# Kernel optimization log

Measured on AMD Instinct MI355X. Metric: run time of the kernel, lower is better.

Reference implementation:

```python
import jax, jax.numpy as jnp
import numpy as np

DIM, EXP = 512, 16
INTERNAL = DIM * EXP  # 8192
BATCH, SEQ = 2, 2048


def setup_inputs() -> dict:
    key = jax.random.key(0)
    ks = jax.random.split(key, 8)
    s = 0.02
    return {
        "x": jax.random.normal(ks[0], (BATCH, SEQ, DIM), jnp.float32),
        "W_dt_w": jax.random.normal(ks[1], (INTERNAL, DIM), jnp.float32) * s,
        "W_dt_b": jnp.zeros((INTERNAL,), jnp.float32),
        "W_B_w": jax.random.normal(ks[2], (INTERNAL, DIM), jnp.float32) * s,
        "W_B_b": jnp.zeros((INTERNAL,), jnp.float32),
        "W_C_w": jax.random.normal(ks[3], (INTERNAL, DIM), jnp.float32) * s,
        "W_C_b": jnp.zeros((INTERNAL,), jnp.float32),
        "W_V_w": jax.random.normal(ks[4], (INTERNAL, DIM), jnp.float32) * s,
        "W_V_b": jnp.zeros((INTERNAL,), jnp.float32),
        # A_log = -rand(internal): negative for stability, as in torch init
        "A_log": -jax.random.uniform(ks[5], (INTERNAL,), jnp.float32),
        "W_out_w": jax.random.normal(ks[6], (DIM, INTERNAL), jnp.float32) * s,
        "W_out_b": jnp.zeros((DIM,), jnp.float32),
    }


def _scan_combine(c1, c2):
    # semi-separable recurrence h_t = a_t * h_{t-1} + b_t, as associative op
    a1, b1 = c1
    a2, b2 = c2
    return a2 * a1, a2 * b1 + b2


def reference(x, W_dt_w, W_dt_b, W_B_w, W_B_b, W_C_w, W_C_b,
              W_V_w, W_V_b, A_log, W_out_w, W_out_b):
    # Featurizer10: discretized SSM features. Shapes: x [b,s,d] -> [b,s,n]
    dt = jax.nn.softplus(jnp.einsum('bsd,nd->bsn', x, W_dt_w) + W_dt_b)
    A_bar = jnp.exp(dt * A_log)                                  # S: [b,s,n]
    B_bar = dt * (jnp.einsum('bsd,nd->bsn', x, W_B_w) + W_B_b)   # B: [b,s,n]
    C = jnp.einsum('bsd,nd->bsn', x, W_C_w) + W_C_b              # C: [b,s,n]
    V = jnp.einsum('bsd,nd->bsn', x, W_V_w) + W_V_b              # V: [b,s,n]
    # Token mixing: h_t = A_bar_t * h_{t-1} + B_bar_t * V_t (parallel scan)
    u = B_bar * V
    _, h = jax.lax.associative_scan(_scan_combine, (A_bar, u), axis=1)
    y = C * h                                                    # [b,s,n]
    # Output projection back to model dim
    return jnp.einsum('bsn,dn->bsd', y, W_out_w) + W_out_b
```

## Files before the change

### kernel.cpp

```cpp
#include <hip/hip_runtime.h>

#define DIMK 512
#define NCH  8192
#define MTOT 4096
#define SEQL 2048
#define KS   8

typedef __attribute__((ext_vector_type(8))) short bf16x8;
typedef __attribute__((ext_vector_type(4))) float f32x4;

__device__ __forceinline__ unsigned short f2bf(float f) {
  unsigned int u = __float_as_uint(f);
  u += 0x7fffu + ((u >> 16) & 1u);
  return (unsigned short)(u >> 16);
}
__device__ __forceinline__ float bf2f(unsigned short v) {
  return __uint_as_float(((unsigned int)v) << 16);
}

struct CvtArgs {
  const float* src[6];
  unsigned short* dst[6];
  int cum[7];
};
__global__ __launch_bounds__(256) void cvt_all_kernel(CvtArgs a, int tot) {
  const int stride = gridDim.x * 256;
  for (int i = blockIdx.x * 256 + threadIdx.x; i < tot; i += stride) {
    int s = 0;
    while (i >= a.cum[s + 1]) ++s;
    const int j = i - a.cum[s];
    const float4* sp = reinterpret_cast<const float4*>(a.src[s]);
    float4 v0 = sp[2 * j], v1 = sp[2 * j + 1];
    union { unsigned short us[8]; uint4 v; } o;
    o.us[0] = f2bf(v0.x); o.us[1] = f2bf(v0.y); o.us[2] = f2bf(v0.z); o.us[3] = f2bf(v0.w);
    o.us[4] = f2bf(v1.x); o.us[5] = f2bf(v1.y); o.us[6] = f2bf(v1.z); o.us[7] = f2bf(v1.w);
    reinterpret_cast<uint4*>(a.dst[s])[j] = o.v;
  }
}

__device__ __forceinline__ int swz(int row, int q) { return q ^ ((row >> 2) & 3); }

#define PLDS_A 4096
#define PLDS_W 8192
#define PLDS   (PLDS_A + PLDS_W)
__global__ __launch_bounds__(256) void proj_kernel(
    const unsigned short* __restrict__ xb,
    const unsigned short* __restrict__ w4,
    const float* __restrict__ b_dt, const float* __restrict__ b_B,
    const float* __restrict__ b_C, const float* __restrict__ b_V,
    const float* __restrict__ A_log,
    unsigned short* __restrict__ vlog,
    unsigned short* __restrict__ u_out,
    unsigned short* __restrict__ c_out)
{
  __shared__ __align__(16) unsigned short lds[3][PLDS];
  const int tid = threadIdx.x;
  const int lane = tid & 63;
  const int wave = tid >> 6;
  const int wr = wave >> 1, wc = wave & 1;
  const int n0 = blockIdx.x * 64;
  const int m0 = blockIdx.y * 128;

  auto stage = [&](int buf, int kt) {
    const int k0 = kt * 32;
    #pragma unroll
    for (int i = 0; i < 2; ++i) {
      int c = i * 256 + tid;
      int row = c >> 2, q = c & 3;
      const unsigned short* g = xb + (size_t)(m0 + row) * DIMK + k0 + swz(row, q) * 8;
      __builtin_amdgcn_global_load_lds(
          (const __attribute__((address_space(1))) void*)g,
          (__attribute__((address_space(3))) void*)&lds[buf][c * 8], 16, 0, 0);
    }
    #pragma unroll
    for (int p = 0; p < 4; ++p) {
      int row = tid >> 2, q = tid & 3;
      const unsigned short* g = w4 + ((size_t)p * NCH + n0 + row) * DIMK + k0 + swz(row, q) * 8;
      __builtin_amdgcn_global_load_lds(
          (const __attribute__((address_space(1))) void*)g,
          (__attribute__((address_space(3))) void*)&lds[buf][PLDS_A + p * 2048 + tid * 8], 16, 0, 0);
    }
  };

  f32x4 acc[4][4][2];
  #pragma unroll
  for (int p = 0; p < 4; ++p)
    #pragma unroll
    for (int fm = 0; fm < 4; ++fm)
      #pragma unroll
      for (int fn = 0; fn < 2; ++fn)
        acc[p][fm][fn] = (f32x4){0.f, 0.f, 0.f, 0.f};

  stage(0, 0);
  stage(1, 1);
  constexpr int NKT = DIMK / 32;
  #pragma unroll 1
  for (int kt = 0; kt < NKT; ++kt) {
    const int buf = kt % 3;
    if (kt < NKT - 1) asm volatile("s_waitcnt vmcnt(6)" ::: "memory");
    else              asm volatile("s_waitcnt vmcnt(0)" ::: "memory");
    __builtin_amdgcn_s_barrier();
    if (kt + 2 < NKT) stage((kt + 2) % 3, kt + 2);

    const int arow = wr * 64 + (lane & 15);
    const int qq = lane >> 4;
    bf16x8 af[4];
    #pragma unroll
    for (int fm = 0; fm < 4; ++fm) {
      const int r = arow + fm * 16;
      af[fm] = *reinterpret_cast<const bf16x8*>(&lds[buf][r * 32 + swz(r, qq) * 8]);
    }
    #pragma unroll
    for (int p = 0; p < 4; ++p) {
      bf16x8 bfr[2];
      #pragma unroll
      for (int fn = 0; fn < 2; ++fn) {
        const int r = wc * 32 + fn * 16 + (lane & 15);
        bfr[fn] = *reinterpret_cast<const bf16x8*>(
            &lds[buf][PLDS_A + p * 2048 + r * 32 + swz(r, qq) * 8]);
      }
      __builtin_amdgcn_s_setprio(1);
      #pragma unroll
      for (int fm = 0; fm < 4; ++fm)
        #pragma unroll
        for (int fn = 0; fn < 2; ++fn)
          acc[p][fm][fn] = __builtin_amdgcn_mfma_f32_16x16x32_bf16(
              af[fm], bfr[fn], acc[p][fm][fn], 0, 0, 0);
      __builtin_amdgcn_s_setprio(0);
    }
    asm volatile("s_waitcnt lgkmcnt(0)" ::: "memory");
  }

  #pragma unroll
  for (int fn = 0; fn < 2; ++fn) {
    const int n = n0 + wc * 32 + fn * 16 + (lane & 15);
    const float vbdt = b_dt[n], vbB = b_B[n], vbC = b_C[n], vbV = b_V[n];
    const float al = A_log[n];
    #pragma unroll
    for (int fm = 0; fm < 4; ++fm) {
      const int mbase = m0 + wr * 64 + fm * 16 + (lane >> 4) * 4;
      #pragma unroll
      for (int r = 0; r < 4; ++r) {
        const size_t off = (size_t)(mbase + r) * NCH + n;
        const float zdt = acc[0][fm][fn][r] + vbdt;
        const float zB  = acc[1][fm][fn][r] + vbB;
        const float zC  = acc[2][fm][fn][r] + vbC;
        const float zV  = acc[3][fm][fn][r] + vbV;
        const float dt = (zdt > 15.f) ? zdt : __logf(1.f + __expf(zdt));
        vlog[off]  = f2bf(dt * al);
        u_out[off] = f2bf(dt * zB * zV);
        c_out[off] = f2bf(zC);
      }
    }
  }
}

#define SCH 16
#define CSTEPS 128
__global__ __launch_bounds__(1024) void scan_kernel(
    const unsigned short* __restrict__ vlog,
    const unsigned short* __restrict__ u_in,
    unsigned short* cy)
{
  __shared__ float Ap[SCH][64], He[SCH][64], H0[SCH][64];
  const int lane = threadIdx.x & 63;
  const int w = threadIdx.x >> 6;
  const int c = blockIdx.x * 64 + lane;
  const size_t base = (size_t)blockIdx.y * SEQL * NCH + (size_t)(w * CSTEPS) * NCH + c;

  {
    const unsigned short* ap = vlog + base;
    const unsigned short* up = u_in + base;
    float h = 0.f, vsum = 0.f;
    #pragma unroll 1
    for (int s = 0; s < CSTEPS; s += 8) {
      float av[8], uv[8];
      #pragma unroll
      for (int i = 0; i < 8; ++i) {
        av[i] = bf2f(ap[(size_t)(s + i) * NCH]);
        uv[i] = bf2f(up[(size_t)(s + i) * NCH]);
      }
      #pragma unroll
      for (int i = 0; i < 8; ++i) {
        vsum += av[i];
        h = fmaf(__expf(av[i]), h, uv[i]);
      }
    }
    Ap[w][lane] = __expf(vsum);
    He[w][lane] = h;
  }
  __syncthreads();
  if (w == 0) {
    float run = 0.f;
    #pragma unroll
    for (int j = 0; j < SCH; ++j) {
      H0[j][lane] = run;
      run = fmaf(Ap[j][lane], run, He[j][lane]);
    }
  }
  __syncthreads();
  {
    const unsigned short* ap = vlog + base;
    const unsigned short* up = u_in + base;
    unsigned short* cp = cy + base;
    float h = H0[w][lane];
    #pragma unroll 1
    for (int s = 0; s < CSTEPS; s += 8) {
      float av[8], uv[8], cv[8];
      #pragma unroll
      for (int i = 0; i < 8; ++i) {
        av[i] = bf2f(ap[(size_t)(s + i) * NCH]);
        uv[i] = bf2f(up[(size_t)(s + i) * NCH]);
        cv[i] = bf2f(cp[(size_t)(s + i) * NCH]);
      }
      #pragma unroll
      for (int i = 0; i < 8; ++i) {
        h = fmaf(__expf(av[i]), h, uv[i]);
        cv[i] *= h;
      }
      #pragma unroll
      for (int i = 0; i < 8; ++i)
        __builtin_nontemporal_store(f2bf(cv[i]), &cp[(size_t)(s + i) * NCH]);
    }
  }
}

#define OLDS_A 4096
#define OLDS_B 2048
#define OLDS   (OLDS_A + OLDS_B)
__global__ __launch_bounds__(256) void outproj_kernel(
    const unsigned short* __restrict__ yb,
    const unsigned short* __restrict__ wout,
    float* __restrict__ partial)
{
  __shared__ __align__(16) unsigned short lds[3][OLDS];
  const int tid = threadIdx.x;
  const int lane = tid & 63;
  const int wave = tid >> 6;
  const int wr = wave >> 1, wc = wave & 1;
  const int m0 = blockIdx.x * 128;
  const int d0 = blockIdx.y * 64;
  const int kbase = blockIdx.z * (NCH / KS);

  auto stage = [&](int buf, int kt) {
    const int k0 = kbase + kt * 32;
    #pragma unroll
    for (int i = 0; i < 2; ++i) {
      int c = i * 256 + tid;
      int row = c >> 2, q = c & 3;
      const unsigned short* g = yb + (size_t)(m0 + row) * NCH + k0 + swz(row, q) * 8;
      __builtin_amdgcn_global_load_lds(
          (const __attribute__((address_space(1))) void*)g,
          (__attribute__((address_space(3))) void*)&lds[buf][c * 8], 16, 0, 0);
    }
    {
      int row = tid >> 2, q = tid & 3;
      const unsigned short* g = wout + (size_t)(d0 + row) * NCH + k0 + swz(row, q) * 8;
      __builtin_amdgcn_global_load_lds(
          (const __attribute__((address_space(1))) void*)g,
          (__attribute__((address_space(3))) void*)&lds[buf][OLDS_A + tid * 8], 16, 0, 0);
    }
  };

  f32x4 acc[4][2];
  #pragma unroll
  for (int fm = 0; fm < 4; ++fm)
    #pragma unroll
    for (int fn = 0; fn < 2; ++fn) acc[fm][fn] = (f32x4){0.f, 0.f, 0.f, 0.f};

  stage(0, 0);
  stage(1, 1);
  constexpr int NKT = (NCH / KS) / 32;
  #pragma unroll 1
  for (int kt = 0; kt < NKT; ++kt) {
    const int buf = kt % 3;
    if (kt < NKT - 1) asm volatile("s_waitcnt vmcnt(3)" ::: "memory");
    else              asm volatile("s_waitcnt vmcnt(0)" ::: "memory");
    __builtin_amdgcn_s_barrier();
    if (kt + 2 < NKT) stage((kt + 2) % 3, kt + 2);

    const int qq = lane >> 4;
    bf16x8 af[4], bfr[2];
    #pragma unroll
    for (int fm = 0; fm < 4; ++fm) {
      const int r = wr * 64 + fm * 16 + (lane & 15);
      af[fm] = *reinterpret_cast<const bf16x8*>(&lds[buf][r * 32 + swz(r, qq) * 8]);
    }
    #pragma unroll
    for (int fn = 0; fn < 2; ++fn) {
      const int r = wc * 32 + fn * 16 + (lane & 15);
      bfr[fn] = *reinterpret_cast<const bf16x8*>(
          &lds[buf][OLDS_A + r * 32 + swz(r, qq) * 8]);
    }
    __builtin_amdgcn_s_setprio(1);
    #pragma unroll
    for (int fm = 0; fm < 4; ++fm)
      #pragma unroll
      for (int fn = 0; fn < 2; ++fn)
        acc[fm][fn] = __builtin_amdgcn_mfma_f32_16x16x32_bf16(
            af[fm], bfr[fn], acc[fm][fn], 0, 0, 0);
    __builtin_amdgcn_s_setprio(0);
    asm volatile("s_waitcnt lgkmcnt(0)" ::: "memory");
  }

  float* pout = partial + (size_t)blockIdx.z * MTOT * DIMK;
  #pragma unroll
  for (int fn = 0; fn < 2; ++fn) {
    const int d = d0 + wc * 32 + fn * 16 + (lane & 15);
    #pragma unroll
    for (int fm = 0; fm < 4; ++fm) {
      const int mbase = m0 + wr * 64 + fm * 16 + (lane >> 4) * 4;
      #pragma unroll
      for (int r = 0; r < 4; ++r)
        __builtin_nontemporal_store(acc[fm][fn][r],
                                    &pout[(size_t)(mbase + r) * DIMK + d]);
    }
  }
}

__global__ __launch_bounds__(256) void reduce_kernel(
    const float* __restrict__ p, const float* __restrict__ bias,
    float* __restrict__ out)
{
  const int i = blockIdx.x * 256 + threadIdx.x;
  const float4* p4 = reinterpret_cast<const float4*>(p);
  float4 s = p4[i];
  #pragma unroll
  for (int k = 1; k < KS; ++k) {
    float4 t = p4[(size_t)k * (MTOT * DIMK / 4) + i];
    s.x += t.x; s.y += t.y; s.z += t.z; s.w += t.w;
  }
  const float4 b = reinterpret_cast<const float4*>(bias)[i & 127];
  s.x += b.x; s.y += b.y; s.z += b.z; s.w += b.w;
  reinterpret_cast<float4*>(out)[i] = s;
}

extern "C" void kernel_launch(void* const* d_in, const int* in_sizes, int n_in,
                              void* d_out, int out_size, void* d_ws, size_t ws_size,
                              hipStream_t stream) {
  const float* x    = (const float*)d_in[0];
  const float* Wdt  = (const float*)d_in[1];
  const float* bdt  = (const float*)d_in[2];
  const float* WB   = (const float*)d_in[3];
  const float* bB   = (const float*)d_in[4];
  const float* WC   = (const float*)d_in[5];
  const float* bC   = (const float*)d_in[6];
  const float* WV   = (const float*)d_in[7];
  const float* bV   = (const float*)d_in[8];
  const float* Alog = (const float*)d_in[9];
  const float* Wout = (const float*)d_in[10];
  const float* bout = (const float*)d_in[11];
  float* out = (float*)d_out;

  char* ws = (char*)d_ws;
  unsigned short* woutb = (unsigned short*)(ws);
  unsigned short* xb    = (unsigned short*)(ws + 8388608);
  unsigned short* w4    = (unsigned short*)(ws + 12582912);
  char* dyn = ws + 46137344;
  const size_t csz = (size_t)MTOT * NCH * 2;
  unsigned short* vlog = (unsigned short*)(dyn);
  unsigned short* u_b  = (unsigned short*)(dyn + csz);
  unsigned short* cy   = (unsigned short*)(dyn + 2 * csz);
  float* partial = (float*)vlog;

  CvtArgs ca;
  ca.src[0] = x;    ca.dst[0] = xb;
  ca.src[1] = Wdt;  ca.dst[1] = w4 + 0 * 4194304;
  ca.src[2] = WB;   ca.dst[2] = w4 + 1 * 4194304;
  ca.src[3] = WC;   ca.dst[3] = w4 + 2 * 4194304;
  ca.src[4] = WV;   ca.dst[4] = w4 + 3 * 4194304;
  ca.src[5] = Wout; ca.dst[5] = woutb;
  ca.cum[0] = 0;        ca.cum[1] = 262144;  ca.cum[2] = 786432;
  ca.cum[3] = 1310720;  ca.cum[4] = 1835008; ca.cum[5] = 2359296;
  ca.cum[6] = 2883584;
  cvt_all_kernel<<<2048, 256, 0, stream>>>(ca, 2883584);

  proj_kernel<<<dim3(NCH / 64, MTOT / 128), 256, 0, stream>>>(
      xb, w4, bdt, bB, bC, bV, Alog, vlog, u_b, cy);
  scan_kernel<<<dim3(NCH / 64, 2), 1024, 0, stream>>>(vlog, u_b, cy);
  outproj_kernel<<<dim3(MTOT / 128, DIMK / 64, KS), 256, 0, stream>>>(
      cy, woutb, partial);
  reduce_kernel<<<MTOT * DIMK / 4 / 256, 256, 0, stream>>>(partial, bout, out);
}
```

Before: 495.7 us.

## Pack scan inputs into one word, remap proj blocks per XCD, halve split-K

The projection kernel now writes log-decay and u as one packed 32-bit word, so the scan reads a single interleaved stream instead of two separate bf16 arrays. The projection grid is flattened to 1D and remapped so that blocks sharing the same weight columns land on the same XCD, which should improve L2 reuse. The out-projection split-K factor drops from 8 to 4, which halves the partial buffer traffic and reduce work but leaves fewer blocks. Nontemporal stores are also replaced with plain stores.

New measurement: 503.8 us. Within noise of the previous version (+1.6%).

```diff
diff --git a/kernel.cpp b/kernel.cpp
--- a/kernel.cpp
+++ b/kernel.cpp
@@ -4,10 +4,11 @@
 #define NCH  8192
 #define MTOT 4096
 #define SEQL 2048
-#define KS   8
+#define KS   4
 
 typedef __attribute__((ext_vector_type(8))) short bf16x8;
 typedef __attribute__((ext_vector_type(4))) float f32x4;
+typedef unsigned int uint32;
 
 __device__ __forceinline__ unsigned short f2bf(float f) {
   unsigned int u = __float_as_uint(f);
@@ -49,8 +50,7 @@
     const float* __restrict__ b_dt, const float* __restrict__ b_B,
     const float* __restrict__ b_C, const float* __restrict__ b_V,
     const float* __restrict__ A_log,
-    unsigned short* __restrict__ vlog,
-    unsigned short* __restrict__ u_out,
+    uint32* __restrict__ au,
     unsigned short* __restrict__ c_out)
 {
   __shared__ __align__(16) unsigned short lds[3][PLDS];
@@ -58,8 +58,10 @@
   const int lane = tid & 63;
   const int wave = tid >> 6;
   const int wr = wave >> 1, wc = wave & 1;
-  const int n0 = blockIdx.x * 64;
-  const int m0 = blockIdx.y * 128;
+  const int id = blockIdx.x;
+  const int xcd = id & 7, j = id >> 3;
+  const int n0 = ((j >> 5) * 8 + xcd) * 64;
+  const int m0 = (j & 31) * 128;
 
   auto stage = [&](int buf, int kt) {
     const int k0 = kt * 32;
@@ -147,8 +149,7 @@
         const float zC  = acc[2][fm][fn][r] + vbC;
         const float zV  = acc[3][fm][fn][r] + vbV;
         const float dt = (zdt > 15.f) ? zdt : __logf(1.f + __expf(zdt));
-        vlog[off]  = f2bf(dt * al);
-        u_out[off] = f2bf(dt * zB * zV);
+        au[off] = ((uint32)f2bf(dt * al) << 16) | (uint32)f2bf(dt * zB * zV);
         c_out[off] = f2bf(zC);
       }
     }
@@ -158,8 +159,7 @@
 #define SCH 16
 #define CSTEPS 128
 __global__ __launch_bounds__(1024) void scan_kernel(
-    const unsigned short* __restrict__ vlog,
-    const unsigned short* __restrict__ u_in,
+    const uint32* __restrict__ au,
     unsigned short* cy)
 {
   __shared__ float Ap[SCH][64], He[SCH][64], H0[SCH][64];
@@ -169,21 +169,19 @@
   const size_t base = (size_t)blockIdx.y * SEQL * NCH + (size_t)(w * CSTEPS) * NCH + c;
 
   {
-    const unsigned short* ap = vlog + base;
-    const unsigned short* up = u_in + base;
+    const uint32* ap = au + base;
     float h = 0.f, vsum = 0.f;
     #pragma unroll 1
     for (int s = 0; s < CSTEPS; s += 8) {
-      float av[8], uv[8];
+      uint32 wv[8];
+      #pragma unroll
+      for (int i = 0; i < 8; ++i) wv[i] = ap[(size_t)(s + i) * NCH];
       #pragma unroll
       for (int i = 0; i < 8; ++i) {
-        av[i] = bf2f(ap[(size_t)(s + i) * NCH]);
-        uv[i] = bf2f(up[(size_t)(s + i) * NCH]);
-      }
-      #pragma unroll
-      for (int i = 0; i < 8; ++i) {
-        vsum += av[i];
-        h = fmaf(__expf(av[i]), h, uv[i]);
+        const float av = bf2f((unsigned short)(wv[i] >> 16));
+        const float uv = bf2f((unsigned short)(wv[i] & 0xffff));
+        vsum += av;
+        h = fmaf(__expf(av), h, uv);
       }
     }
     Ap[w][lane] = __expf(vsum);
@@ -193,34 +191,34 @@
   if (w == 0) {
     float run = 0.f;
     #pragma unroll
-    for (int j = 0; j < SCH; ++j) {
-      H0[j][lane] = run;
-      run = fmaf(Ap[j][lane], run, He[j][lane]);
+    for (int jj = 0; jj < SCH; ++jj) {
+      H0[jj][lane] = run;
+      run = fmaf(Ap[jj][lane], run, He[jj][lane]);
     }
   }
   __syncthreads();
   {
-    const unsigned short* ap = vlog + base;
-    const unsigned short* up = u_in + base;
+    const uint32* ap = au + base;
     unsigned short* cp = cy + base;
     float h = H0[w][lane];
     #pragma unroll 1
     for (int s = 0; s < CSTEPS; s += 8) {
-      float av[8], uv[8], cv[8];
+      uint32 wv[8];
+      float cv[8];
       #pragma unroll
       for (int i = 0; i < 8; ++i) {
-        av[i] = bf2f(ap[(size_t)(s + i) * NCH]);
-        uv[i] = bf2f(up[(size_t)(s + i) * NCH]);
+        wv[i] = ap[(size_t)(s + i) * NCH];
         cv[i] = bf2f(cp[(size_t)(s + i) * NCH]);
       }
       #pragma unroll
       for (int i = 0; i < 8; ++i) {
-        h = fmaf(__expf(av[i]), h, uv[i]);
+        const float av = bf2f((unsigned short)(wv[i] >> 16));
+        const float uv = bf2f((unsigned short)(wv[i] & 0xffff));
+        h = fmaf(__expf(av), h, uv);
         cv[i] *= h;
       }
       #pragma unroll
-      for (int i = 0; i < 8; ++i)
-        __builtin_nontemporal_store(f2bf(cv[i]), &cp[(size_t)(s + i) * NCH]);
+      for (int i = 0; i < 8; ++i) cp[(size_t)(s + i) * NCH] = f2bf(cv[i]);
     }
   }
 }
@@ -312,8 +310,7 @@
       const int mbase = m0 + wr * 64 + fm * 16 + (lane >> 4) * 4;
       #pragma unroll
       for (int r = 0; r < 4; ++r)
-        __builtin_nontemporal_store(acc[fm][fn][r],
-                                    &pout[(size_t)(mbase + r) * DIMK + d]);
+        pout[(size_t)(mbase + r) * DIMK + d] = acc[fm][fn][r];
     }
   }
 }
@@ -357,11 +354,9 @@
   unsigned short* xb    = (unsigned short*)(ws + 8388608);
   unsigned short* w4    = (unsigned short*)(ws + 12582912);
   char* dyn = ws + 46137344;
-  const size_t csz = (size_t)MTOT * NCH * 2;
-  unsigned short* vlog = (unsigned short*)(dyn);
-  unsigned short* u_b  = (unsigned short*)(dyn + csz);
-  unsigned short* cy   = (unsigned short*)(dyn + 2 * csz);
-  float* partial = (float*)vlog;
+  uint32*         au  = (uint32*)(dyn);
+  unsigned short* cy  = (unsigned short*)(dyn + (size_t)MTOT * NCH * 4);
+  float* partial = (float*)au;
 
   CvtArgs ca;
   ca.src[0] = x;    ca.dst[0] = xb;
@@ -375,9 +370,9 @@
   ca.cum[6] = 2883584;
   cvt_all_kernel<<<2048, 256, 0, stream>>>(ca, 2883584);
 
-  proj_kernel<<<dim3(NCH / 64, MTOT / 128), 256, 0, stream>>>(
-      xb, w4, bdt, bB, bC, bV, Alog, vlog, u_b, cy);
-  scan_kernel<<<dim3(NCH / 64, 2), 1024, 0, stream>>>(vlog, u_b, cy);
+  proj_kernel<<<4096, 256, 0, stream>>>(
+      xb, w4, bdt, bB, bC, bV, Alog, au, cy);
+  scan_kernel<<<dim3(NCH / 64, 2), 1024, 0, stream>>>(au, cy);
   outproj_kernel<<<dim3(MTOT / 128, DIMK / 64, KS), 256, 0, stream>>>(
       cy, woutb, partial);
   reduce_kernel<<<MTOT * DIMK / 4 / 256, 256, 0, stream>>>(partial, bout, out);
```
